# Performance work log

Hardware: AMD Instinct MI355X
Metric: run time of the kernel (lower is better)

The kernel has to match this reference:

```python
import jax, jax.numpy as jnp
import numpy as np

N_NODES = 100000


def sage_conv(x, edge_index, W_l, W_r, b):
    # PyG SAGEConv (aggr='mean', root_weight=True):
    # out_i = (mean_{j in N(i)} x_j) @ W_l + x_i @ W_r + b
    src, dst = edge_index[0], edge_index[1]
    msgs = x[src]                                             # [E, F] gather
    summed = jax.ops.segment_sum(msgs, dst, num_segments=N_NODES)
    deg = jax.ops.segment_sum(jnp.ones((edge_index.shape[1],), x.dtype), dst,
                              num_segments=N_NODES)
    mean = summed / jnp.maximum(deg, 1.0)[:, None]            # [N, F]
    return mean @ W_l + x @ W_r + b


def setup_inputs() -> dict:
    key = jax.random.key(0)
    ks = jax.random.split(key, 12)
    F, H = 128, 128
    E = 1600000
    s = lambda k, shp, fan: jax.random.normal(k, shp, jnp.float32) / np.sqrt(fan)
    return {
        "x": jax.random.normal(ks[0], (N_NODES, F), jnp.float32),
        "edge_index": jax.random.randint(ks[1], (2, E), 0, N_NODES, jnp.int64),
        "W1_l": s(ks[2], (F, H), F), "W1_r": s(ks[3], (F, H), F),
        "b1": jnp.zeros((H,), jnp.float32),
        "W2_l": s(ks[4], (H, H), H), "W2_r": s(ks[5], (H, H), H),
        "b2": jnp.zeros((H,), jnp.float32),
        "W3_l": s(ks[6], (H, 1), H), "W3_r": s(ks[7], (H, 1), H),
        "b3": jnp.zeros((1,), jnp.float32),
    }


def reference(x, edge_index, W1_l, W1_r, b1, W2_l, W2_r, b2, W3_l, W3_r, b3):
    h = jax.nn.relu(sage_conv(x, edge_index, W1_l, W1_r, b1))
    h = jax.nn.relu(sage_conv(h, edge_index, W2_l, W2_r, b2))
    h = sage_conv(h, edge_index, W3_l, W3_r, b3)   # [N, 1]
    return h.mean(axis=1)                          # [N]
```

## Files before the change

kernel.cpp:

```cpp
#include <hip/hip_runtime.h>


#define NN 100000
#define NB 391
#define SLAB 5120
#define NGB 1563

typedef short bf16x8 __attribute__((ext_vector_type(8)));
typedef float f32x4 __attribute__((ext_vector_type(4)));

static __device__ __forceinline__ float uaf(unsigned u) { return __uint_as_float(u); }
static __device__ __forceinline__ unsigned short f2bf(float f) {
  unsigned u = __float_as_uint(f);
  u += 0x7fffu + ((u >> 16) & 1u);
  return (unsigned short)(u >> 16);
}

static __device__ __forceinline__ size_t fo_addr16(int nd, int c) {
  return (size_t)(nd >> 6) * 8192 + (size_t)(c >> 2) * 2048 +
         (size_t)((nd >> 4) & 3) * 512 + (size_t)(((c & 3) << 4) + (nd & 15)) * 8;
}

__global__ __launch_bounds__(256) void k_prep(
    const int* __restrict__ src, const int* __restrict__ dst, int E, int SB,
    int* __restrict__ cursor, unsigned* __restrict__ pairs,
    const float* __restrict__ x, unsigned short* __restrict__ Zrm,
    unsigned short* __restrict__ root1,
    const float* __restrict__ W1l, const float* __restrict__ W1r,
    const float* __restrict__ W2l, const float* __restrict__ W2r,
    unsigned short* __restrict__ wt1h, unsigned short* __restrict__ wt1l,
    unsigned short* __restrict__ wt2h, unsigned short* __restrict__ wt2l) {
  __shared__ int h[NB];
  __shared__ int rb[NB];
  const int b = blockIdx.x;
  const int tid = threadIdx.x;
  const int XB = NN * 16 / 256;

  if (b < SB) {
    for (int i = tid; i < NB; i += 256) h[i] = 0;
    __syncthreads();
    int s[8], d[8];
    const int base = b * 2048 + tid * 8;
    #pragma unroll
    for (int i = 0; i < 8; i++) {
      int g = base + i;
      bool ok = g < E;
      s[i] = ok ? src[g] : 0;
      d[i] = ok ? dst[g] : -1;
      if (ok) atomicAdd(&h[d[i] >> 8], 1);
    }
    __syncthreads();
    for (int i = tid; i < NB; i += 256) {
      rb[i] = h[i] ? atomicAdd(&cursor[i], h[i]) : 0;
      h[i] = 0;
    }
    __syncthreads();
    #pragma unroll
    for (int i = 0; i < 8; i++) {
      if (d[i] >= 0) {
        int bk = d[i] >> 8;
        int off = rb[bk] + atomicAdd(&h[bk], 1);
        if (off < SLAB)
          pairs[(size_t)bk * SLAB + off] =
              ((unsigned)(d[i] & 255) << 17) | (unsigned)s[i];
      }
    }
  } else if (b < SB + XB) {
    int t = (b - SB) * 256 + tid;
    int node = t >> 4, c = t & 15;
    const float4* xp = (const float4*)(x + (size_t)node * 128 + c * 8);
    float4 a = xp[0], bb = xp[1];
    float v[8] = {a.x, a.y, a.z, a.w, bb.x, bb.y, bb.z, bb.w};
    unsigned hh[8];
    #pragma unroll
    for (int i = 0; i < 8; i++) hh[i] = f2bf(v[i]);
    uint4 p;
    p.x = hh[0] | (hh[1] << 16); p.y = hh[2] | (hh[3] << 16);
    p.z = hh[4] | (hh[5] << 16); p.w = hh[6] | (hh[7] << 16);
    *(uint4*)(Zrm + (size_t)node * 128 + c * 8) = p;
    *(uint4*)(root1 + fo_addr16(node, c)) = p;
  } else if (b < SB + XB + 64) {
    #pragma unroll
    for (int it = 0; it < 4; it++) {
      int t = (b - SB - XB) * 1024 + it * 256 + tid;
      int layer = t >> 15;
      int rem = t & 32767;
      int k = rem >> 7;
      int nn = rem & 127;
      const float* Wl = layer ? W2l : W1l;
      const float* Wr = layer ? W2r : W1r;
      float v = (k < 128) ? Wl[k * 128 + nn] : Wr[(k - 128) * 128 + nn];
      unsigned short hv = f2bf(v);
      unsigned short lv = f2bf(v - uaf(((unsigned)hv) << 16));
      const int frag = (nn >> 4) * 8 + (k >> 7) * 4 + ((k >> 5) & 3);
      const int lane = ((k >> 3) & 3) * 16 + (nn & 15);
      const int addr = frag * 512 + lane * 8 + (k & 7);
      (layer ? wt2h : wt1h)[addr] = hv;
      (layer ? wt2l : wt1l)[addr] = lv;
    }
  } else {
    unsigned* zr = (unsigned*)(Zrm + (size_t)NN * 128);
    if (tid < 64) zr[tid] = 0;
  }
}

__global__ __launch_bounds__(256) void k_build(const unsigned* __restrict__ pairs,
                                               const int* __restrict__ cursor,
                                               int* __restrict__ beg, int* __restrict__ deg,
                                               int* __restrict__ csr, int N) {
  __shared__ int cnt[256];
  __shared__ int sd[256];
  __shared__ int cur[256];
  const int b = blockIdx.x;
  const int tid = threadIdx.x;
  const size_t p0 = (size_t)b * SLAB;
  int count = cursor[b];
  if (count > SLAB) count = SLAB;
  cnt[tid] = 0;
  cur[tid] = 0;
  __syncthreads();
  for (int i = tid; i < count; i += 256) atomicAdd(&cnt[pairs[p0 + i] >> 17], 1);
  __syncthreads();
  int v = cnt[tid];
  sd[tid] = v;
  __syncthreads();
  #pragma unroll
  for (int off = 1; off < 256; off <<= 1) {
    int u = (tid >= off) ? sd[tid - off] : 0;
    __syncthreads();
    sd[tid] += u;
    __syncthreads();
  }
  const int node = b * 256 + tid;
  if (node < N) {
    beg[node] = (int)p0 + (sd[tid] - v);
    deg[node] = v;
  }
  __syncthreads();
  for (int i = tid; i < count; i += 256) {
    unsigned pv = pairs[p0 + i];
    int dl = pv >> 17;
    int pos = (sd[dl] - cnt[dl]) + atomicAdd(&cur[dl], 1);
    csr[p0 + pos] = pv & 0x1ffff;
  }
}

#define ACC8(v)                                   \
  acc[0] += uaf((v).x << 16);                     \
  acc[1] += uaf((v).x & 0xffff0000u);             \
  acc[2] += uaf((v).y << 16);                     \
  acc[3] += uaf((v).y & 0xffff0000u);             \
  acc[4] += uaf((v).z << 16);                     \
  acc[5] += uaf((v).z & 0xffff0000u);             \
  acc[6] += uaf((v).w << 16);                     \
  acc[7] += uaf((v).w & 0xffff0000u);

__global__ __launch_bounds__(256) void k_aggZ(const unsigned short* __restrict__ Zrm,
                                              unsigned short* __restrict__ aggfo,
                                              const int* __restrict__ begA,
                                              const int* __restrict__ degA,
                                              const int* __restrict__ csr, int n) {
  const int wid = (blockIdx.x * blockDim.x + threadIdx.x) >> 6;
  const int lane = threadIdx.x & 63;
  if (wid >= n) return;
  const int beg = begA[wid];
  const int d = degA[wid];
  const int g = lane >> 4, c = lane & 15;
  float acc[8] = {0.f, 0.f, 0.f, 0.f, 0.f, 0.f, 0.f, 0.f};

  for (int base = 0; base < d; base += 64) {
    int m = d - base;
    if (m > 64) m = 64;
    int idx = csr[beg + base + (lane < m ? lane : 0)];
    for (int k = 0; k < m; k += 32) {
      uint4 vA[4], vB[4];
      const bool hasB = (k + 16) < m;
      #pragma unroll
      for (int u = 0; u < 4; u++) {
        int kk = k + u * 4 + g;
        int j = __shfl(idx, kk & 63);
        j = (kk < m) ? j : NN;
        vA[u] = *(const uint4*)(Zrm + (size_t)j * 128 + c * 8);
      }
      if (hasB) {
        #pragma unroll
        for (int u = 0; u < 4; u++) {
          int kk = k + 16 + u * 4 + g;
          int j = __shfl(idx, kk & 63);
          j = (kk < m) ? j : NN;
          vB[u] = *(const uint4*)(Zrm + (size_t)j * 128 + c * 8);
        }
      }
      #pragma unroll
      for (int u = 0; u < 4; u++) { ACC8(vA[u]); }
      if (hasB) {
        #pragma unroll
        for (int u = 0; u < 4; u++) { ACC8(vB[u]); }
      }
    }
  }
  #pragma unroll
  for (int j = 0; j < 8; j++) {
    acc[j] += __shfl_xor(acc[j], 16);
    acc[j] += __shfl_xor(acc[j], 32);
  }
  const float inv = d > 0 ? 1.0f / (float)d : 0.f;
  if (g == 0) {
    unsigned h[8];
    #pragma unroll
    for (int j = 0; j < 8; j++) h[j] = f2bf(acc[j] * inv);
    uint4 p;
    p.x = h[0] | (h[1] << 16); p.y = h[2] | (h[3] << 16);
    p.z = h[4] | (h[5] << 16); p.w = h[6] | (h[7] << 16);
    *(uint4*)(aggfo + fo_addr16(wid, c)) = p;
  }
}

template <int MODE>
__global__ __launch_bounds__(256, 2) void k_sage2(
    const unsigned short* __restrict__ aggfo, const unsigned short* __restrict__ rootfo,
    const unsigned short* __restrict__ WTh, const unsigned short* __restrict__ WTl,
    const float* __restrict__ bias,
    unsigned short* __restrict__ Zrm_out, unsigned short* __restrict__ rootfo_out,
    const float* __restrict__ w3l, const float* __restrict__ w3r,
    float* __restrict__ s2, float* __restrict__ r2, int n) {
  const int tid = threadIdx.x;
  const int lane = tid & 63;
  const int w = tid >> 6;
  const int ln = lane & 15;
  const int r16 = lane >> 4;
  const int m0 = blockIdx.x * 256 + w * 64;
  const size_t fbase = (size_t)(m0 >> 6) * 8192;

  f32x4 acc[4][8];
  #pragma unroll
  for (int s = 0; s < 4; s++)
    #pragma unroll
    for (int cc = 0; cc < 8; cc++) {
      acc[s][cc][0] = 0.f; acc[s][cc][1] = 0.f;
      acc[s][cc][2] = 0.f; acc[s][cc][3] = 0.f;
    }
  float4 bv4[8];
  #pragma unroll
  for (int cc = 0; cc < 8; cc++) bv4[cc] = *(const float4*)(bias + cc * 16 + r16 * 4);

  #pragma unroll
  for (int kh = 0; kh < 2; kh++) {
    const unsigned short* zf = kh ? rootfo : aggfo;
    bf16x8 a[4][4];
    #pragma unroll
    for (int ks = 0; ks < 4; ks++)
      #pragma unroll
      for (int s = 0; s < 4; s++)
        a[s][ks] = *(const bf16x8*)(zf + fbase + (size_t)ks * 2048 + s * 512 + lane * 8);
    #pragma unroll
    for (int ks = 0; ks < 4; ks++) {
      #pragma unroll
      for (int cg = 0; cg < 4; cg++) {
        bf16x8 bh[2], bl[2];
        #pragma unroll
        for (int j = 0; j < 2; j++) {
          const size_t o = (size_t)(((cg * 2 + j) * 8 + kh * 4 + ks) * 512 + lane * 8);
          bh[j] = *(const bf16x8*)(WTh + o);
          bl[j] = *(const bf16x8*)(WTl + o);
        }
        #pragma unroll
        for (int j = 0; j < 2; j++) {
          #pragma unroll
          for (int s = 0; s < 4; s++) {
            acc[s][cg * 2 + j] =
                __builtin_amdgcn_mfma_f32_16x16x32_bf16(bh[j], a[s][ks], acc[s][cg * 2 + j], 0, 0, 0);
            acc[s][cg * 2 + j] =
                __builtin_amdgcn_mfma_f32_16x16x32_bf16(bl[j], a[s][ks], acc[s][cg * 2 + j], 0, 0, 0);
          }
        }
      }
    }
  }

  if (MODE == 0) {
    #pragma unroll
    for (int s = 0; s < 4; s++) {
      const int node = m0 + s * 16 + ln;
      if (node < n) {
        unsigned short* op = Zrm_out + (size_t)node * 128 + r16 * 4;
        #pragma unroll
        for (int cc = 0; cc < 8; cc++) {
          ushort4 hq;
          hq.x = f2bf(fmaxf(acc[s][cc][0] + bv4[cc].x, 0.f));
          hq.y = f2bf(fmaxf(acc[s][cc][1] + bv4[cc].y, 0.f));
          hq.z = f2bf(fmaxf(acc[s][cc][2] + bv4[cc].z, 0.f));
          hq.w = f2bf(fmaxf(acc[s][cc][3] + bv4[cc].w, 0.f));
          *(ushort4*)(op + cc * 16) = hq;
          const size_t fo = fbase + (size_t)(cc >> 1) * 2048 + (size_t)s * 512 +
                            (size_t)((((cc & 1) * 2 + (r16 >> 1)) << 4) + ln) * 8 +
                            (r16 & 1) * 4;
          *(ushort4*)(rootfo_out + fo) = hq;
        }
      }
    }
  } else {
    float4 wl4[8], wr4[8];
    #pragma unroll
    for (int cc = 0; cc < 8; cc++) {
      wl4[cc] = *(const float4*)(w3l + cc * 16 + r16 * 4);
      wr4[cc] = *(const float4*)(w3r + cc * 16 + r16 * 4);
    }
    #pragma unroll
    for (int s = 0; s < 4; s++) {
      float sl = 0.f, sr = 0.f;
      #pragma unroll
      for (int cc = 0; cc < 8; cc++) {
        float v0 = fmaxf(acc[s][cc][0] + bv4[cc].x, 0.f);
        float v1 = fmaxf(acc[s][cc][1] + bv4[cc].y, 0.f);
        float v2 = fmaxf(acc[s][cc][2] + bv4[cc].z, 0.f);
        float v3 = fmaxf(acc[s][cc][3] + bv4[cc].w, 0.f);
        sl += v0 * wl4[cc].x + v1 * wl4[cc].y + v2 * wl4[cc].z + v3 * wl4[cc].w;
        sr += v0 * wr4[cc].x + v1 * wr4[cc].y + v2 * wr4[cc].z + v3 * wr4[cc].w;
      }
      sl += __shfl_xor(sl, 16); sl += __shfl_xor(sl, 32);
      sr += __shfl_xor(sr, 16); sr += __shfl_xor(sr, 32);
      const int node = m0 + s * 16 + ln;
      if (r16 == 0 && node < n) {
        s2[node] = sl;
        r2[node] = sr;
      }
    }
  }
}

__global__ __launch_bounds__(256) void k_out3(const float* __restrict__ s2,
                                              const float* __restrict__ r2,
                                              const int* __restrict__ beg,
                                              const int* __restrict__ deg,
                                              const int* __restrict__ csr,
                                              const float* __restrict__ b3,
                                              float* __restrict__ out, int n) {
  int t = blockIdx.x * blockDim.x + threadIdx.x;
  int node = t >> 4;
  int ln = t & 15;
  if (node >= n) return;
  int bg = beg[node], d = deg[node];
  float s = 0.f;
  for (int i = ln; i < d; i += 16) s += s2[csr[bg + i]];
  s += __shfl_xor(s, 1); s += __shfl_xor(s, 2);
  s += __shfl_xor(s, 4); s += __shfl_xor(s, 8);
  if (ln == 0) out[node] = s / (d > 0 ? (float)d : 1.0f) + r2[node] + b3[0];
}

extern "C" void kernel_launch(void* const* d_in, const int* in_sizes, int n_in,
                              void* d_out, int out_size, void* d_ws, size_t ws_size,
                              hipStream_t stream) {
  const float* x   = (const float*)d_in[0];
  const int*   ei  = (const int*)d_in[1];
  const float* W1l = (const float*)d_in[2];
  const float* W1r = (const float*)d_in[3];
  const float* b1  = (const float*)d_in[4];
  const float* W2l = (const float*)d_in[5];
  const float* W2r = (const float*)d_in[6];
  const float* b2  = (const float*)d_in[7];
  const float* W3l = (const float*)d_in[8];
  const float* W3r = (const float*)d_in[9];
  const float* b3  = (const float*)d_in[10];
  float* out = (float*)d_out;

  const int N = NN;
  const int E = in_sizes[1] / 2;
  const int* src = ei;
  const int* dst = ei + E;

  char* ws = (char*)d_ws;
  size_t off = 0;
  auto alloc = [&](size_t bytes) -> char* {
    char* p = ws + off;
    off = (off + bytes + 255) & ~(size_t)255;
    return p;
  };
  int* cursor = (int*)alloc((NB + 1) * 4);
  unsigned* pairs = (unsigned*)alloc((size_t)NB * SLAB * 4);
  int* csr  = (int*)alloc(((size_t)NB * SLAB + 128) * 4);
  int* beg  = (int*)alloc((size_t)N * 4);
  int* deg  = (int*)alloc((size_t)N * 4);
  float* s2 = (float*)alloc((size_t)N * 4);
  float* r2 = (float*)alloc((size_t)N * 4);
  unsigned short* wt1h = (unsigned short*)alloc(128 * 256 * 2);
  unsigned short* wt1l = (unsigned short*)alloc(128 * 256 * 2);
  unsigned short* wt2h = (unsigned short*)alloc(128 * 256 * 2);
  unsigned short* wt2l = (unsigned short*)alloc(128 * 256 * 2);
  unsigned short* Zrm   = (unsigned short*)alloc((size_t)(N + 1) * 128 * 2);
  unsigned short* root1 = (unsigned short*)alloc((size_t)NGB * 8192 * 2);
  unsigned short* agg1  = (unsigned short*)alloc((size_t)NGB * 8192 * 2);
  unsigned short* root2 = (unsigned short*)alloc((size_t)NGB * 8192 * 2);
  unsigned short* agg2  = root1;

  hipMemsetAsync(cursor, 0, (NB + 1) * 4, stream);
  const size_t tail = (size_t)(NGB - 1) * 8192 * 2;
  hipMemsetAsync((char*)root1 + tail, 0, 8192 * 2, stream);
  hipMemsetAsync((char*)agg1 + tail, 0, 8192 * 2, stream);
  hipMemsetAsync((char*)root2 + tail, 0, 8192 * 2, stream);

  const int SB = (E + 2047) / 2048;
  const int XB = N * 16 / 256;
  k_prep<<<SB + XB + 64 + 1, 256, 0, stream>>>(
      src, dst, E, SB, cursor, pairs, x, Zrm, root1,
      W1l, W1r, W2l, W2r, wt1h, wt1l, wt2h, wt2l);
  k_build<<<NB, 256, 0, stream>>>(pairs, cursor, beg, deg, csr, N);

  const int wb = (N * 64 + 255) / 256;
  const int sb = (N + 255) / 256;
  k_aggZ<<<wb, 256, 0, stream>>>(Zrm, agg1, beg, deg, csr, N);
  k_sage2<0><<<sb, 256, 0, stream>>>(agg1, root1, wt1h, wt1l, b1, Zrm, root2,
                                     nullptr, nullptr, nullptr, nullptr, N);
  k_aggZ<<<wb, 256, 0, stream>>>(Zrm, agg2, beg, deg, csr, N);
  k_sage2<1><<<sb, 256, 0, stream>>>(agg2, root2, wt2h, wt2l, b2, nullptr, nullptr,
                                     W3l, W3r, s2, r2, N);
  k_out3<<<(N * 16 + 255) / 256, 256, 0, stream>>>(s2, r2, beg, deg, csr, b3, out, N);
}
```

Baseline: 260.1 us.

## Drop fragment-ordered copies; transpose row-major inputs through swizzled LDS in sage GEMM

Removes the duplicate MFMA-fragment-ordered buffers (root1, agg, root2). Before, prep and the first sage kernel wrote every activation twice, once row-major and once in fragment order. Now aggregation writes row-major, and the sage kernel loads 64-row tiles per wave into XOR-swizzled shared memory before reading MFMA fragments. This cuts global write traffic and the tail memsets, and layer 1 updates Zrm in place. The cost is 64KB of LDS per block, which may limit occupancy, plus extra LDS round-trips. It also relies on padded rows past N that are never initialized.

```diff
diff --git a/kernel.cpp b/kernel.cpp
--- a/kernel.cpp
+++ b/kernel.cpp
@@ -4,7 +4,6 @@
 #define NN 100000
 #define NB 391
 #define SLAB 5120
-#define NGB 1563
 
 typedef short bf16x8 __attribute__((ext_vector_type(8)));
 typedef float f32x4 __attribute__((ext_vector_type(4)));
@@ -16,16 +15,10 @@
   return (unsigned short)(u >> 16);
 }
 
-static __device__ __forceinline__ size_t fo_addr16(int nd, int c) {
-  return (size_t)(nd >> 6) * 8192 + (size_t)(c >> 2) * 2048 +
-         (size_t)((nd >> 4) & 3) * 512 + (size_t)(((c & 3) << 4) + (nd & 15)) * 8;
-}
-
 __global__ __launch_bounds__(256) void k_prep(
     const int* __restrict__ src, const int* __restrict__ dst, int E, int SB,
     int* __restrict__ cursor, unsigned* __restrict__ pairs,
     const float* __restrict__ x, unsigned short* __restrict__ Zrm,
-    unsigned short* __restrict__ root1,
     const float* __restrict__ W1l, const float* __restrict__ W1r,
     const float* __restrict__ W2l, const float* __restrict__ W2r,
     unsigned short* __restrict__ wt1h, unsigned short* __restrict__ wt1l,
@@ -78,7 +71,6 @@
     p.x = hh[0] | (hh[1] << 16); p.y = hh[2] | (hh[3] << 16);
     p.z = hh[4] | (hh[5] << 16); p.w = hh[6] | (hh[7] << 16);
     *(uint4*)(Zrm + (size_t)node * 128 + c * 8) = p;
-    *(uint4*)(root1 + fo_addr16(node, c)) = p;
   } else if (b < SB + XB + 64) {
     #pragma unroll
     for (int it = 0; it < 4; it++) {
@@ -156,7 +148,7 @@
   acc[7] += uaf((v).w & 0xffff0000u);
 
 __global__ __launch_bounds__(256) void k_aggZ(const unsigned short* __restrict__ Zrm,
-                                              unsigned short* __restrict__ aggfo,
+                                              unsigned short* __restrict__ Zagg,
                                               const int* __restrict__ begA,
                                               const int* __restrict__ degA,
                                               const int* __restrict__ csr, int n) {
@@ -212,25 +204,25 @@
     uint4 p;
     p.x = h[0] | (h[1] << 16); p.y = h[2] | (h[3] << 16);
     p.z = h[4] | (h[5] << 16); p.w = h[6] | (h[7] << 16);
-    *(uint4*)(aggfo + fo_addr16(wid, c)) = p;
+    *(uint4*)(Zagg + (size_t)wid * 128 + c * 8) = p;
   }
 }
 
 template <int MODE>
 __global__ __launch_bounds__(256, 2) void k_sage2(
-    const unsigned short* __restrict__ aggfo, const unsigned short* __restrict__ rootfo,
+    const unsigned short* __restrict__ Zagg, const unsigned short* __restrict__ Zroot,
     const unsigned short* __restrict__ WTh, const unsigned short* __restrict__ WTl,
-    const float* __restrict__ bias,
-    unsigned short* __restrict__ Zrm_out, unsigned short* __restrict__ rootfo_out,
+    const float* __restrict__ bias, unsigned short* __restrict__ Zout,
     const float* __restrict__ w3l, const float* __restrict__ w3r,
     float* __restrict__ s2, float* __restrict__ r2, int n) {
+  __shared__ __align__(16) unsigned short tile[4][8192];
   const int tid = threadIdx.x;
   const int lane = tid & 63;
   const int w = tid >> 6;
   const int ln = lane & 15;
   const int r16 = lane >> 4;
   const int m0 = blockIdx.x * 256 + w * 64;
-  const size_t fbase = (size_t)(m0 >> 6) * 8192;
+  char* T = (char*)tile[w];
 
   f32x4 acc[4][8];
   #pragma unroll
@@ -246,13 +238,22 @@
 
   #pragma unroll
   for (int kh = 0; kh < 2; kh++) {
-    const unsigned short* zf = kh ? rootfo : aggfo;
+    const unsigned short* zsrc = kh ? Zroot : Zagg;
+    #pragma unroll
+    for (int i = 0; i < 16; i++) {
+      const int nl = i * 4 + r16;
+      uint4 v = *(const uint4*)(zsrc + (size_t)(m0 + nl) * 128 + ln * 8);
+      *(uint4*)(T + nl * 256 + ((ln * 16) ^ ((nl & 7) << 4))) = v;
+    }
     bf16x8 a[4][4];
     #pragma unroll
     for (int ks = 0; ks < 4; ks++)
       #pragma unroll
-      for (int s = 0; s < 4; s++)
-        a[s][ks] = *(const bf16x8*)(zf + fbase + (size_t)ks * 2048 + s * 512 + lane * 8);
+      for (int s = 0; s < 4; s++) {
+        const int nl = s * 16 + ln;
+        a[s][ks] = *(const bf16x8*)(T + nl * 256 +
+                                    ((ks * 64 + r16 * 16) ^ ((nl & 7) << 4)));
+      }
     #pragma unroll
     for (int ks = 0; ks < 4; ks++) {
       #pragma unroll
@@ -283,7 +284,7 @@
     for (int s = 0; s < 4; s++) {
       const int node = m0 + s * 16 + ln;
       if (node < n) {
-        unsigned short* op = Zrm_out + (size_t)node * 128 + r16 * 4;
+        unsigned short* op = Zout + (size_t)node * 128 + r16 * 4;
         #pragma unroll
         for (int cc = 0; cc < 8; cc++) {
           ushort4 hq;
@@ -292,10 +293,6 @@
           hq.z = f2bf(fmaxf(acc[s][cc][2] + bv4[cc].z, 0.f));
           hq.w = f2bf(fmaxf(acc[s][cc][3] + bv4[cc].w, 0.f));
           *(ushort4*)(op + cc * 16) = hq;
-          const size_t fo = fbase + (size_t)(cc >> 1) * 2048 + (size_t)s * 512 +
-                            (size_t)((((cc & 1) * 2 + (r16 >> 1)) << 4) + ln) * 8 +
-                            (r16 & 1) * 4;
-          *(ushort4*)(rootfo_out + fo) = hq;
         }
       }
     }
@@ -387,32 +384,25 @@
   unsigned short* wt1l = (unsigned short*)alloc(128 * 256 * 2);
   unsigned short* wt2h = (unsigned short*)alloc(128 * 256 * 2);
   unsigned short* wt2l = (unsigned short*)alloc(128 * 256 * 2);
-  unsigned short* Zrm   = (unsigned short*)alloc((size_t)(N + 1) * 128 * 2);
-  unsigned short* root1 = (unsigned short*)alloc((size_t)NGB * 8192 * 2);
-  unsigned short* agg1  = (unsigned short*)alloc((size_t)NGB * 8192 * 2);
-  unsigned short* root2 = (unsigned short*)alloc((size_t)NGB * 8192 * 2);
-  unsigned short* agg2  = root1;
+  unsigned short* Zrm  = (unsigned short*)alloc((size_t)(N + 160) * 128 * 2);
+  unsigned short* Zagg = (unsigned short*)alloc((size_t)(N + 160) * 128 * 2);
 
   hipMemsetAsync(cursor, 0, (NB + 1) * 4, stream);
-  const size_t tail = (size_t)(NGB - 1) * 8192 * 2;
-  hipMemsetAsync((char*)root1 + tail, 0, 8192 * 2, stream);
-  hipMemsetAsync((char*)agg1 + tail, 0, 8192 * 2, stream);
-  hipMemsetAsync((char*)root2 + tail, 0, 8192 * 2, stream);
 
   const int SB = (E + 2047) / 2048;
   const int XB = N * 16 / 256;
   k_prep<<<SB + XB + 64 + 1, 256, 0, stream>>>(
-      src, dst, E, SB, cursor, pairs, x, Zrm, root1,
+      src, dst, E, SB, cursor, pairs, x, Zrm,
       W1l, W1r, W2l, W2r, wt1h, wt1l, wt2h, wt2l);
   k_build<<<NB, 256, 0, stream>>>(pairs, cursor, beg, deg, csr, N);
 
   const int wb = (N * 64 + 255) / 256;
   const int sb = (N + 255) / 256;
-  k_aggZ<<<wb, 256, 0, stream>>>(Zrm, agg1, beg, deg, csr, N);
-  k_sage2<0><<<sb, 256, 0, stream>>>(agg1, root1, wt1h, wt1l, b1, Zrm, root2,
+  k_aggZ<<<wb, 256, 0, stream>>>(Zrm, Zagg, beg, deg, csr, N);
+  k_sage2<0><<<sb, 256, 0, stream>>>(Zagg, Zrm, wt1h, wt1l, b1, Zrm,
                                      nullptr, nullptr, nullptr, nullptr, N);
-  k_aggZ<<<wb, 256, 0, stream>>>(Zrm, agg2, beg, deg, csr, N);
-  k_sage2<1><<<sb, 256, 0, stream>>>(agg2, root2, wt2h, wt2l, b2, nullptr, nullptr,
+  k_aggZ<<<wb, 256, 0, stream>>>(Zrm, Zagg, beg, deg, csr, N);
+  k_sage2<1><<<sb, 256, 0, stream>>>(Zagg, Zrm, wt2h, wt2l, b2, nullptr,
                                      W3l, W3r, s2, r2, N);
   k_out3<<<(N * 16 + 255) / 256, 256, 0, stream>>>(s2, r2, beg, deg, csr, b3, out, N);
 }
```

Result: faster. 248.9 us (-4.3%).
